# Optimization experiments

Measured on AMD Instinct MI355X. Metric: run time of the kernel, lower is better.

The kernel has to match this reference:

```python
import jax, jax.numpy as jnp
import numpy as np

NUM_CLASSES = 7

def setup_inputs() -> dict:
    key = jax.random.key(0)
    k1, k2, k3 = jax.random.split(key, 3)
    B = 4_000_000
    logit = jax.random.normal(k1, (B, NUM_CLASSES), dtype=jnp.float32)
    label = jax.random.randint(k2, (B,), 0, 2, dtype=jnp.int32)
    repr_num = jax.random.randint(k3, (B, 3), 0, NUM_CLASSES, dtype=jnp.int64)
    return {"logit": logit, "label": label, "repr_num": repr_num}

def reference(logit, label, repr_num) -> jnp.ndarray:
    B = logit.shape[0]
    logit = logit.reshape(B, -1)  # [B, 7]
    # membership mask: mask[i, j] = (j in repr_num[i])  -> [B, 7]
    mask = jnp.any(repr_num[:, :, None] == jnp.arange(NUM_CLASSES, dtype=repr_num.dtype), axis=1)
    # target margin: 1.0 for positive samples, 0.0 otherwise
    target = jnp.where(label == 1, jnp.float32(1.0), jnp.float32(0.0))[:, None]  # [B, 1]
    d = logit - target  # [B, 7]
    elem = jnp.where(mask, jnp.abs(d), jax.nn.relu(d))
    return jnp.sum(elem)
```

## Files before the change

kernel.cpp:

```cpp
#include <hip/hip_runtime.h>


#define NUM_CLASSES 7

__global__ __launch_bounds__(256) void hinge_sum_kernel(
    const float* __restrict__ logit,
    const int* __restrict__ label,
    const int* __restrict__ repr_num,
    float* __restrict__ out,
    int B)
{
    int tid = blockIdx.x * blockDim.x + threadIdx.x;
    int stride = gridDim.x * blockDim.x;

    float acc = 0.0f;
    for (int i = tid; i < B; i += stride) {
        int r0 = repr_num[3 * i + 0];
        int r1 = repr_num[3 * i + 1];
        int r2 = repr_num[3 * i + 2];
        unsigned mbits = (1u << r0) | (1u << r1) | (1u << r2);

        float target = (label[i] == 1) ? 1.0f : 0.0f;

        const float* lrow = logit + (size_t)i * NUM_CLASSES;
        #pragma unroll
        for (int j = 0; j < NUM_CLASSES; ++j) {
            float d = lrow[j] - target;
            float v = ((mbits >> j) & 1u) ? fabsf(d) : fmaxf(d, 0.0f);
            acc += v;
        }
    }

    #pragma unroll
    for (int off = 32; off > 0; off >>= 1)
        acc += __shfl_down(acc, off, 64);

    __shared__ float wave_sums[4];
    int lane = threadIdx.x & 63;
    int wid  = threadIdx.x >> 6;
    if (lane == 0) wave_sums[wid] = acc;
    __syncthreads();

    if (threadIdx.x == 0) {
        float s = wave_sums[0] + wave_sums[1] + wave_sums[2] + wave_sums[3];
        atomicAdd(out, s);
    }
}

extern "C" void kernel_launch(void* const* d_in, const int* in_sizes, int n_in,
                              void* d_out, int out_size, void* d_ws, size_t ws_size,
                              hipStream_t stream) {
    const float* logit    = (const float*)d_in[0];
    const int*   label    = (const int*)d_in[1];
    const int*   repr_num = (const int*)d_in[2];
    float*       out      = (float*)d_out;

    int B = in_sizes[1];

    hipMemsetAsync(out, 0, sizeof(float), stream);

    int threads = 256;
    int blocks  = 2048;
    hinge_sum_kernel<<<blocks, threads, 0, stream>>>(logit, label, repr_num, out, B);
}
```

Measured before the change: 208.2 us.

## Stage row tiles through LDS with coalesced float4 loads

Each block now loads a 512-row tile of logits, labels and repr indices into shared memory using fully coalesced 16-byte vector loads, then computes per-row hinge terms from LDS. This targets the strided, poorly coalesced per-thread row reads of 7 floats and 3 ints. The grid is also reduced to 1792 blocks. It adds two barriers per tile and about 22 KB of LDS per block, which limits occupancy, and there is no overlap between loading and computing.

```diff
diff --git a/kernel.cpp b/kernel.cpp
--- a/kernel.cpp
+++ b/kernel.cpp
@@ -1,34 +1,58 @@
 #include <hip/hip_runtime.h>
 
 
-#define NUM_CLASSES 7
+#define NCLS   7
+#define T_ROWS 512
 
 __global__ __launch_bounds__(256) void hinge_sum_kernel(
-    const float* __restrict__ logit,
-    const int* __restrict__ label,
-    const int* __restrict__ repr_num,
+    const float4* __restrict__ logit4,
+    const int4*  __restrict__ label4,
+    const int4*  __restrict__ repr4,
     float* __restrict__ out,
-    int B)
+    int B, int ntiles)
 {
-    int tid = blockIdx.x * blockDim.x + threadIdx.x;
-    int stride = gridDim.x * blockDim.x;
+    __shared__ float s_logit[T_ROWS * NCLS];
+    __shared__ int   s_label[T_ROWS];
+    __shared__ int   s_repr [T_ROWS * 3];
 
+    const int tid = threadIdx.x;
     float acc = 0.0f;
-    for (int i = tid; i < B; i += stride) {
-        int r0 = repr_num[3 * i + 0];
-        int r1 = repr_num[3 * i + 1];
-        int r2 = repr_num[3 * i + 2];
-        unsigned mbits = (1u << r0) | (1u << r1) | (1u << r2);
 
-        float target = (label[i] == 1) ? 1.0f : 0.0f;
+    for (int tile = blockIdx.x; tile < ntiles; tile += gridDim.x) {
+        const int row_base = tile * T_ROWS;
+        const int rows = min(T_ROWS, B - row_base);
 
-        const float* lrow = logit + (size_t)i * NUM_CLASSES;
-        #pragma unroll
-        for (int j = 0; j < NUM_CLASSES; ++j) {
-            float d = lrow[j] - target;
-            float v = ((mbits >> j) & 1u) ? fabsf(d) : fmaxf(d, 0.0f);
-            acc += v;
+        const int nlog4 = (rows * NCLS) / 4;
+        const float4* gl = logit4 + ((size_t)row_base * NCLS) / 4;
+        for (int k = tid; k < nlog4; k += 256)
+            ((float4*)s_logit)[k] = gl[k];
+
+        const int nlab4 = (rows + 3) / 4;
+        const int4* glb = label4 + row_base / 4;
+        for (int k = tid; k < nlab4; k += 256)
+            ((int4*)s_label)[k] = glb[k];
+
+        const int nrep4 = (rows * 3) / 4;
+        const int4* grp = repr4 + ((size_t)row_base * 3) / 4;
+        for (int k = tid; k < nrep4; k += 256)
+            ((int4*)s_repr)[k] = grp[k];
+
+        __syncthreads();
+
+        for (int r = tid; r < rows; r += 256) {
+            float tgt = (s_label[r] == 1) ? 1.0f : 0.0f;
+            int a = s_repr[3 * r + 0];
+            int b = s_repr[3 * r + 1];
+            int c = s_repr[3 * r + 2];
+            unsigned m = (1u << a) | (1u << b) | (1u << c);
+            #pragma unroll
+            for (int j = 0; j < NCLS; ++j) {
+                float d = s_logit[r * NCLS + j] - tgt;
+                acc += ((m >> j) & 1u) ? fabsf(d) : fmaxf(d, 0.0f);
+            }
         }
+
+        __syncthreads();
     }
 
     #pragma unroll
@@ -41,7 +65,7 @@
     if (lane == 0) wave_sums[wid] = acc;
     __syncthreads();
 
-    if (threadIdx.x == 0) {
+    if (tid == 0) {
         float s = wave_sums[0] + wave_sums[1] + wave_sums[2] + wave_sums[3];
         atomicAdd(out, s);
     }
@@ -50,16 +74,17 @@
 extern "C" void kernel_launch(void* const* d_in, const int* in_sizes, int n_in,
                               void* d_out, int out_size, void* d_ws, size_t ws_size,
                               hipStream_t stream) {
-    const float* logit    = (const float*)d_in[0];
-    const int*   label    = (const int*)d_in[1];
-    const int*   repr_num = (const int*)d_in[2];
-    float*       out      = (float*)d_out;
+    const float4* logit4 = (const float4*)d_in[0];
+    const int4*   label4 = (const int4*)d_in[1];
+    const int4*   repr4  = (const int4*)d_in[2];
+    float*        out    = (float*)d_out;
 
     int B = in_sizes[1];
+    int ntiles = (B + T_ROWS - 1) / T_ROWS;
 
     hipMemsetAsync(out, 0, sizeof(float), stream);
 
     int threads = 256;
-    int blocks  = 2048;
-    hinge_sum_kernel<<<blocks, threads, 0, stream>>>(logit, label, repr_num, out, B);
+    int blocks  = 1792;
+    hinge_sum_kernel<<<blocks, threads, 0, stream>>>(logit4, label4, repr4, out, B, ntiles);
 }
```

Result: slower. 220.7 us (+6.0%).

## Stage row tiles into LDS with async global_load_lds double buffering

Applied to the files above, without the earlier changes.

Replaces per-thread strided global loads with one wave issuing 16-byte global_load_lds copies of 256-row tiles (logits, labels, repr indices) into a double-buffered LDS region, prefetching the next tile while the current one is consumed. The goal is fully coalesced reads of the 7-float and 3-int row strides and overlap of memory with compute. The atomicAdd is replaced by per-block partials and a second single-block kernel that reduces them and handles the tail rows, which drops the memset. The cost is an extra launch, two barriers per tile, and only one wave issuing loads.

```diff
diff --git a/kernel.cpp b/kernel.cpp
--- a/kernel.cpp
+++ b/kernel.cpp
@@ -1,34 +1,89 @@
 #include <hip/hip_runtime.h>
+#include <stdint.h>
 
 
-#define NUM_CLASSES 7
+#define NCLS 7
+#define T_ROWS 256
+#define LOG_B  (T_ROWS * NCLS * 4)
+#define LAB_B  (T_ROWS * 4)
+#define REP_B  (T_ROWS * 3 * 4)
+#define TILE_B (LOG_B + LAB_B + REP_B)
+#define NBLK 1792
 
-__global__ __launch_bounds__(256) void hinge_sum_kernel(
-    const float* __restrict__ logit,
-    const int* __restrict__ label,
-    const int* __restrict__ repr_num,
-    float* __restrict__ out,
-    int B)
+typedef const __attribute__((address_space(1))) void g_void;
+typedef __attribute__((address_space(3))) void l_void;
+
+__device__ __forceinline__ void stage16(const char* g, char* l) {
+    __builtin_amdgcn_global_load_lds((g_void*)g, (l_void*)l, 16, 0, 0);
+}
+
+__global__ __launch_bounds__(256) void hinge_stage_kernel(
+    const char* __restrict__ glog,
+    const char* __restrict__ glab,
+    const char* __restrict__ grep,
+    float* __restrict__ partials,
+    int ntiles)
 {
-    int tid = blockIdx.x * blockDim.x + threadIdx.x;
-    int stride = gridDim.x * blockDim.x;
+    __shared__ char lds[2 * TILE_B];
+
+    const int tid  = threadIdx.x;
+    const int lane = tid & 63;
+    const int wid  = tid >> 6;
+    const int lofs = lane * 16;
 
     float acc = 0.0f;
-    for (int i = tid; i < B; i += stride) {
-        int r0 = repr_num[3 * i + 0];
-        int r1 = repr_num[3 * i + 1];
-        int r2 = repr_num[3 * i + 2];
-        unsigned mbits = (1u << r0) | (1u << r1) | (1u << r2);
+    int cur = 0;
 
-        float target = (label[i] == 1) ? 1.0f : 0.0f;
+    const int t0 = blockIdx.x;
 
-        const float* lrow = logit + (size_t)i * NUM_CLASSES;
+    if (t0 < ntiles && wid == 0) {
+        const char* gl = glog + (size_t)t0 * LOG_B + lofs;
+        const char* gb = glab + (size_t)t0 * LAB_B + lofs;
+        const char* gr = grep + (size_t)t0 * REP_B + lofs;
+        char* L = lds;
         #pragma unroll
-        for (int j = 0; j < NUM_CLASSES; ++j) {
-            float d = lrow[j] - target;
-            float v = ((mbits >> j) & 1u) ? fabsf(d) : fmaxf(d, 0.0f);
-            acc += v;
+        for (int c = 0; c < 7; ++c) stage16(gl + c * 1024, L + c * 1024);
+        stage16(gb, L + LOG_B);
+        #pragma unroll
+        for (int c = 0; c < 3; ++c) stage16(gr + c * 1024, L + LOG_B + LAB_B + c * 1024);
+    }
+
+    for (int t = t0; t < ntiles; t += NBLK) {
+        const int tn = t + NBLK;
+        if (wid == 0) {
+            if (tn < ntiles) {
+                const char* gl = glog + (size_t)tn * LOG_B + lofs;
+                const char* gb = glab + (size_t)tn * LAB_B + lofs;
+                const char* gr = grep + (size_t)tn * REP_B + lofs;
+                char* L = lds + (cur ^ 1) * TILE_B;
+                #pragma unroll
+                for (int c = 0; c < 7; ++c) stage16(gl + c * 1024, L + c * 1024);
+                stage16(gb, L + LOG_B);
+                #pragma unroll
+                for (int c = 0; c < 3; ++c) stage16(gr + c * 1024, L + LOG_B + LAB_B + c * 1024);
+                asm volatile("s_waitcnt vmcnt(11)" ::: "memory");
+            } else {
+                asm volatile("s_waitcnt vmcnt(0)" ::: "memory");
+            }
         }
+        __builtin_amdgcn_s_barrier();
+
+        {
+            const float* sl = (const float*)(lds + cur * TILE_B);
+            const int*   sb = (const int*)(lds + cur * TILE_B + LOG_B);
+            const int*   sr = (const int*)(lds + cur * TILE_B + LOG_B + LAB_B);
+            const int r = tid;
+            float tgt = (sb[r] == 1) ? 1.0f : 0.0f;
+            unsigned m = (1u << sr[3 * r]) | (1u << sr[3 * r + 1]) | (1u << sr[3 * r + 2]);
+            #pragma unroll
+            for (int j = 0; j < NCLS; ++j) {
+                float d = sl[r * NCLS + j] - tgt;
+                acc += ((m >> j) & 1u) ? fabsf(d) : fmaxf(d, 0.0f);
+            }
+        }
+
+        __builtin_amdgcn_s_barrier();
+        cur ^= 1;
     }
 
     #pragma unroll
@@ -36,30 +91,58 @@
         acc += __shfl_down(acc, off, 64);
 
     __shared__ float wave_sums[4];
-    int lane = threadIdx.x & 63;
-    int wid  = threadIdx.x >> 6;
-    if (lane == 0) wave_sums[wid] = acc;
+    if ((tid & 63) == 0) wave_sums[tid >> 6] = acc;
     __syncthreads();
+    if (tid == 0)
+        partials[blockIdx.x] = wave_sums[0] + wave_sums[1] + wave_sums[2] + wave_sums[3];
+}
 
-    if (threadIdx.x == 0) {
-        float s = wave_sums[0] + wave_sums[1] + wave_sums[2] + wave_sums[3];
-        atomicAdd(out, s);
+__global__ __launch_bounds__(256) void reduce_partials_kernel(
+    const float* __restrict__ partials, int n,
+    const float* __restrict__ logit, const int* __restrict__ label,
+    const int* __restrict__ repr, int tail_start, int B,
+    float* __restrict__ out)
+{
+    float a = 0.0f;
+    for (int i = threadIdx.x; i < n; i += 256)
+        a += partials[i];
+
+    for (int i = tail_start + threadIdx.x; i < B; i += 256) {
+        float tgt = (label[i] == 1) ? 1.0f : 0.0f;
+        unsigned m = (1u << repr[3 * i]) | (1u << repr[3 * i + 1]) | (1u << repr[3 * i + 2]);
+        #pragma unroll
+        for (int j = 0; j < NCLS; ++j) {
+            float d = logit[i * NCLS + j] - tgt;
+            a += ((m >> j) & 1u) ? fabsf(d) : fmaxf(d, 0.0f);
+        }
     }
+
+    #pragma unroll
+    for (int off = 32; off > 0; off >>= 1)
+        a += __shfl_down(a, off, 64);
+
+    __shared__ float wave_sums[4];
+    if ((threadIdx.x & 63) == 0) wave_sums[threadIdx.x >> 6] = a;
+    __syncthreads();
+    if (threadIdx.x == 0)
+        out[0] = wave_sums[0] + wave_sums[1] + wave_sums[2] + wave_sums[3];
 }
 
 extern "C" void kernel_launch(void* const* d_in, const int* in_sizes, int n_in,
                               void* d_out, int out_size, void* d_ws, size_t ws_size,
                               hipStream_t stream) {
-    const float* logit    = (const float*)d_in[0];
-    const int*   label    = (const int*)d_in[1];
-    const int*   repr_num = (const int*)d_in[2];
-    float*       out      = (float*)d_out;
+    const char* glog = (const char*)d_in[0];
+    const char* glab = (const char*)d_in[1];
+    const char* grep = (const char*)d_in[2];
+    float*      out  = (float*)d_out;
+    float*      partials = (float*)d_ws;
 
     int B = in_sizes[1];
+    int ntiles = B / T_ROWS;
+    int tail_start = ntiles * T_ROWS;
 
-    hipMemsetAsync(out, 0, sizeof(float), stream);
-
-    int threads = 256;
-    int blocks  = 2048;
-    hinge_sum_kernel<<<blocks, threads, 0, stream>>>(logit, label, repr_num, out, B);
+    hinge_stage_kernel<<<NBLK, 256, 0, stream>>>(glog, glab, grep, partials, ntiles);
+    reduce_partials_kernel<<<1, 256, 0, stream>>>(
+        partials, NBLK, (const float*)d_in[0], (const int*)d_in[1],
+        (const int*)d_in[2], tail_start, B, out);
 }
```

After: 205.6 us. No clear change (-1.2%).
